# Optimization experiments

Measured on AMD Instinct MI355X. Metric: run time of the kernel, lower is better.

## Reference

```python
import jax, jax.numpy as jnp
import numpy as np

B, S, E, NH = 2, 2048, 1024, 4
HD = E // NH  # 256


def setup_inputs() -> dict:
    key = jax.random.key(0)
    ks = jax.random.split(key, 8)
    return {
        "q": jax.random.normal(ks[0], (B, S, E), jnp.float32),
        "k": jax.random.normal(ks[1], (B, S, E), jnp.float32),
        "v": jax.random.normal(ks[2], (B, S, E), jnp.float32),
        # gate Dense params (kernel zero-init in the module; use small random for a nontrivial baseline)
        "igate_kernel": jax.random.normal(ks[3], (3 * E, NH), jnp.float32) * 0.02,
        "igate_bias": jax.random.normal(ks[4], (NH,), jnp.float32) * 0.1,
        "fgate_kernel": jax.random.normal(ks[5], (3 * E, NH), jnp.float32) * 0.02,
        "fgate_bias": jnp.linspace(3.0, 6.0, NH, dtype=jnp.float32),  # bias_linspace_init
        "rms_scale": jax.random.normal(ks[6], (HD,), jnp.float32) * 0.02,
    }


def _mlstm_head(q, k, v, ig, fg, eps=1e-06):
    # q,k,v: (S, DH); ig, fg: (S, 1)
    s, dh = q.shape
    log_f = jax.nn.log_sigmoid(fg)                       # (S,1)
    cs = jnp.concatenate([jnp.zeros((1, 1), log_f.dtype),
                          jnp.cumsum(log_f, axis=0)], axis=0)  # (S+1,1)
    neg = jnp.asarray(-0.7 * jnp.finfo(cs.dtype).max, cs.dtype)
    log_d = jnp.where(jnp.tri(s, dtype=bool),
                      (cs - cs.T)[1:, 1:] + ig.T, neg)   # (S,S)
    m = jnp.max(log_d, axis=-1, keepdims=True)           # row-wise stabilizer
    d = jnp.exp(log_d - m)
    c = (q @ (k.T / jnp.sqrt(dh))) * d                   # (S,S)
    n = jnp.maximum(jnp.sum(c, axis=-1, keepdims=True), jnp.exp(-m))
    return (c / (n + eps)) @ v                           # (S,DH)


def reference(q, k, v, igate_kernel, igate_bias, fgate_kernel, fgate_bias, rms_scale):
    b, s, e = q.shape
    nh = igate_kernel.shape[1]
    hd = e // nh
    gate_in = jnp.concatenate((q, k, v), axis=-1)                 # (B,S,3E)
    ig = (gate_in @ igate_kernel + igate_bias).swapaxes(-1, -2)[..., None]  # (B,NH,S,1)
    fg = (gate_in @ fgate_kernel + fgate_bias).swapaxes(-1, -2)[..., None]  # (B,NH,S,1)
    qh = q.reshape(b, s, nh, hd).swapaxes(1, 2)                   # (B,NH,S,HD)
    kh = k.reshape(b, s, nh, hd).swapaxes(1, 2)
    vh = v.reshape(b, s, nh, hd).swapaxes(1, 2)
    h = jax.vmap(jax.vmap(_mlstm_head))(qh, kh, vh, ig, fg)      # (B,NH,S,HD)
    # RMSNorm over head_dim with (1+scale)
    var = jnp.mean(jnp.square(h.astype(jnp.float32)), axis=-1, keepdims=True)
    h = (h * jax.lax.rsqrt(var + 1e-06)).astype(h.dtype) * (1.0 + rms_scale)
    return h.swapaxes(1, 2).reshape(b, s, e)
```

## Files before the change

kernel.cpp:

```cpp
#include <hip/hip_runtime.h>
#include <math.h>

static constexpr int B_  = 2;
static constexpr int S_  = 2048;
static constexpr int E_  = 1024;
static constexpr int NH_ = 4;
static constexpr int HD_ = 256;
static constexpr int BH_ = B_ * NH_;

typedef __attribute__((ext_vector_type(8))) _Float16 half8;
typedef __attribute__((ext_vector_type(4))) float    f32x4;
typedef __attribute__((ext_vector_type(4))) _Float16 half4v;

__global__ __launch_bounds__(1024) void prep_kernel(
    const float* __restrict__ q, const float* __restrict__ k, const float* __restrict__ v,
    const float* __restrict__ igk, const float* __restrict__ igb,
    const float* __restrict__ fgk, const float* __restrict__ fgb,
    float* __restrict__ ig_out, float* __restrict__ fg_out,
    _Float16* __restrict__ Qh, _Float16* __restrict__ Kh, _Float16* __restrict__ Vt)
{
    __shared__ __align__(16) char PSM[98304];
    float4* wi = (float4*)PSM;
    float4* wf = wi + 3 * E_;

    const int t = threadIdx.x;
    #pragma unroll
    for (int i = 0; i < 3; ++i) {
        int e = t + 1024 * i;
        wi[e] = ((const float4*)igk)[e];
        wf[e] = ((const float4*)fgk)[e];
    }
    __syncthreads();

    const int wave = t >> 6;
    const int l    = t & 63;
    const int bs   = blockIdx.x * 16 + wave;
    const int b = bs >> 11, s = bs & (S_ - 1);
    const float* qrow = q + (size_t)bs * E_;
    const float* krow = k + (size_t)bs * E_;
    const float* vrow = v + (size_t)bs * E_;

    float accI[4] = {0.f,0.f,0.f,0.f}, accF[4] = {0.f,0.f,0.f,0.f};
    #pragma unroll
    for (int j = 0; j < 48; ++j) {
        const int e = l + 64 * j;
        float g;
        if (j < 16)       g = qrow[e];
        else if (j < 32)  g = krow[e - E_];
        else              g = vrow[e - 2 * E_];
        if (j < 16) {
            int hh = e >> 8, d = e & 255;
            Qh[(((size_t)(b * NH_ + hh)) * S_ + s) * HD_ + d] = (_Float16)(g * 0.0625f);
        } else if (j < 32) {
            int e2 = e - E_; int hh = e2 >> 8, d = e2 & 255;
            Kh[(((size_t)(b * NH_ + hh)) * S_ + s) * HD_ + d] = (_Float16)g;
        }
        float4 wiv = wi[e];
        float4 wfv = wf[e];
        accI[0] = fmaf(g, wiv.x, accI[0]); accI[1] = fmaf(g, wiv.y, accI[1]);
        accI[2] = fmaf(g, wiv.z, accI[2]); accI[3] = fmaf(g, wiv.w, accI[3]);
        accF[0] = fmaf(g, wfv.x, accF[0]); accF[1] = fmaf(g, wfv.y, accF[1]);
        accF[2] = fmaf(g, wfv.z, accF[2]); accF[3] = fmaf(g, wfv.w, accF[3]);
    }
    #pragma unroll
    for (int m = 1; m < 64; m <<= 1) {
        #pragma unroll
        for (int h = 0; h < 4; ++h) {
            accI[h] += __shfl_xor(accI[h], m);
            accF[h] += __shfl_xor(accF[h], m);
        }
    }
    if (l == 0) {
        #pragma unroll
        for (int h = 0; h < 4; ++h) {
            ig_out[((size_t)(b * NH_ + h)) * S_ + s] = accI[h] + igb[h];
            fg_out[((size_t)(b * NH_ + h)) * S_ + s] = accF[h] + fgb[h];
        }
    }

    __syncthreads();
    {
        float (*tile)[65] = (float(*)[65])(PSM + (t >> 8) * 16640);
        const int tid = t & 255;
        const int m  = blockIdx.x * 4 + (t >> 8);
        const int bh = m & 7;
        const int sb = (m >> 3) & 31;
        const int db = m >> 8;
        const int bb = bh >> 2, hh = bh & 3;
        const int j4 = (tid & 15) * 4;
        const int i0 = tid >> 4;
        const float* src = v + ((size_t)(bb * S_ + sb * 64)) * E_ + hh * HD_ + db * 64;
        #pragma unroll
        for (int p = 0; p < 4; ++p) {
            int i = i0 + p * 16;
            float4 val = *(const float4*)(src + (size_t)i * E_ + j4);
            tile[i][j4] = val.x; tile[i][j4+1] = val.y; tile[i][j4+2] = val.z; tile[i][j4+3] = val.w;
        }
        __syncthreads();
        const int s4 = (tid & 15) * 4;
        const int d0 = tid >> 4;
        _Float16* dst = Vt + ((size_t)bh * HD_ + db * 64) * S_ + sb * 64;
        #pragma unroll
        for (int p = 0; p < 4; ++p) {
            int d = d0 + p * 16;
            half4v pk;
            pk.x = (_Float16)tile[s4][d];   pk.y = (_Float16)tile[s4+1][d];
            pk.z = (_Float16)tile[s4+2][d]; pk.w = (_Float16)tile[s4+3][d];
            *(half4v*)(dst + (size_t)d * S_ + s4) = pk;
        }
    }
}

static constexpr int KSS = 264;
static constexpr int VSS = 72;
static constexpr int PBS = 72;
static constexpr int OFF_VS  = 64 * KSS * 2;
static constexpr int OFF_PB  = OFF_VS + 256 * VSS * 2;
static constexpr int OFF_RSE = OFF_PB + 2 * 16 * PBS * 2;
static constexpr int OFF_SSE = OFF_RSE + 512;
static constexpr int OFF_AMM = OFF_SSE + 512;
static constexpr int OFF_G   = OFF_AMM + S_ * 4;
static constexpr int OFF_M   = OFF_G   + S_ * 4;
static constexpr int SMB     = OFF_M   + S_ * 4;

__global__ __launch_bounds__(512, 2) void mlstm_kernel(
    const _Float16* __restrict__ Qh, const _Float16* __restrict__ Kh,
    const _Float16* __restrict__ Vt,
    const float* __restrict__ ig, const float* __restrict__ fg,
    const float* __restrict__ rms_scale, float* __restrict__ out)
{
    __shared__ __align__(16) char SMEM[SMB];
    _Float16* Ks    = (_Float16*)SMEM;
    _Float16* Vs    = (_Float16*)(SMEM + OFF_VS);
    _Float16* Pb    = (_Float16*)(SMEM + OFF_PB);
    float*    rsumE = (float*)(SMEM + OFF_RSE);
    float*    ssE   = (float*)(SMEM + OFF_SSE);
    float*    sAmM  = (float*)(SMEM + OFF_AMM);
    float*    sG    = (float*)(SMEM + OFF_G);
    float*    sM    = (float*)(SMEM + OFF_M);

    const int z  = blockIdx.x;
    const int bh = z & 7;
    const int u  = z >> 3;
    const int b  = bh >> 2, h = bh & 3;
    const int t  = threadIdx.x;
    const int w  = t >> 6;
    const int l  = t & 63;
    const int col  = l & 15;
    const int quad = l >> 4;
    const int qo   = quad * 8;
    const int rw   = w >> 2;
    const int cq   = w & 3;

    {
        float* sc = (float*)SMEM;
        const float* fgp = fg + (size_t)bh * S_;
        const float* igp = ig + (size_t)bh * S_;
        float ls[4];
        float run = 0.f;
        #pragma unroll
        for (int i = 0; i < 4; ++i) {
            float x = fgp[t * 4 + i];
            float lg = (x >= 0.f) ? -log1pf(expf(-x)) : (x - log1pf(expf(x)));
            run += lg;
            ls[i] = run;
        }
        sc[t] = run;
        __syncthreads();
        for (int off = 1; off < 512; off <<= 1) {
            float vv = (t >= off) ? sc[t - off] : 0.f;
            __syncthreads();
            sc[t] += vv;
            __syncthreads();
        }
        float excl = sc[t] - run;
        float A[4], g[4], gm[4];
        #pragma unroll
        for (int i = 0; i < 4; ++i) A[i] = excl + ls[i];
        float rmax = -__builtin_inff();
        #pragma unroll
        for (int i = 0; i < 4; ++i) {
            g[i] = igp[t * 4 + i] - A[i];
            rmax = fmaxf(rmax, g[i]);
            gm[i] = rmax;
        }
        __syncthreads();
        sc[t] = rmax;
        __syncthreads();
        for (int off = 1; off < 512; off <<= 1) {
            float vv = (t >= off) ? sc[t - off] : -__builtin_inff();
            __syncthreads();
            sc[t] = fmaxf(sc[t], vv);
            __syncthreads();
        }
        float exm = (t == 0) ? -__builtin_inff() : sc[t - 1];
        #pragma unroll
        for (int i = 0; i < 4; ++i) {
            float cm = fmaxf(exm, gm[i]);
            float Mi = A[i] + cm;
            sAmM[t * 4 + i] = A[i] - Mi;
            sG[t * 4 + i]   = g[i];
            sM[t * 4 + i]   = Mi;
        }
        __syncthreads();
    }

    const _Float16* Qp  = Qh + (size_t)bh * S_ * HD_;
    const _Float16* Kp  = Kh + (size_t)bh * S_ * HD_;
    const _Float16* Vtp = Vt + (size_t)bh * HD_ * S_;
    _Float16* Pbr = Pb + rw * 16 * PBS;

    half8 kpre[4], vpre[4];
    auto issueK = [&](int c0n) {
        #pragma unroll
        for (int i = 0; i < 4; ++i) {
            int p = t + 512 * i;
            int row = p >> 5, ck = p & 31;
            kpre[i] = *(const half8*)(Kp + (size_t)(c0n + row) * HD_ + ck * 8);
        }
    };
    auto issueV = [&](int c0n) {
        #pragma unroll
        for (int i = 0; i < 4; ++i) {
            int p = t + 512 * i;
            int n = p >> 3, ch = p & 7;
            vpre[i] = *(const half8*)(Vtp + (size_t)n * S_ + c0n + ch * 8);
        }
    };

    issueK(0);
    issueV(0);

    for (int pass = 0; pass < 2; ++pass) {
        const int rb = pass ? (63 - u) : u;
        const int rowbase = rb * 32 + rw * 16;

        half8 qf[8];
        #pragma unroll
        for (int kk = 0; kk < 8; ++kk)
            qf[kk] = *(const half8*)(Qp + (size_t)(rowbase + col) * HD_ + kk * 32 + qo);
        float amM[4];
        #pragma unroll
        for (int rr = 0; rr < 4; ++rr) amM[rr] = sAmM[rowbase + quad * 4 + rr];

        f32x4 acc[4];
        #pragma unroll
        for (int nn = 0; nn < 4; ++nn) acc[nn] = (f32x4){0.f, 0.f, 0.f, 0.f};
        float rs[4] = {0.f, 0.f, 0.f, 0.f};

        const int Tt = (rb >> 1) + 1;
        for (int jt = 0; jt < Tt; ++jt) {
            const int c0 = jt << 6;
            __syncthreads();
            #pragma unroll
            for (int i = 0; i < 4; ++i) {
                int p = t + 512 * i;
                int row = p >> 5, ck = p & 31;
                *(half8*)(Ks + row * KSS + ck * 8) = kpre[i];
            }
            #pragma unroll
            for (int i = 0; i < 4; ++i) {
                int p = t + 512 * i;
                int n = p >> 3, ch = p & 7;
                *(half8*)(Vs + n * VSS + ch * 8) = vpre[i];
            }
            __syncthreads();
            if (!(pass == 1 && jt + 1 == Tt)) {
                const int cn = (jt + 1 < Tt) ? (c0 + 64) : 0;
                issueK(cn);
                issueV(cn);
            }
            const float gv = sG[c0 + cq * 16 + col];
            f32x4 sc0 = (f32x4){0.f,0.f,0.f,0.f};
            #pragma unroll
            for (int kk = 0; kk < 8; ++kk) {
                half8 kf = *(const half8*)(Ks + (cq * 16 + col) * KSS + kk * 32 + qo);
                sc0 = __builtin_amdgcn_mfma_f32_16x16x32_f16(qf[kk], kf, sc0, 0, 0, 0);
            }
            #pragma unroll
            for (int rr = 0; rr < 4; ++rr) {
                const int ig_ = rowbase + quad * 4 + rr;
                float e0 = __expf(amM[rr] + gv);
                float p0 = (c0 + cq * 16 + col <= ig_) ? sc0[rr] * e0 : 0.f;
                rs[rr] += p0;
                Pbr[(quad * 4 + rr) * PBS + cq * 16 + col] = (_Float16)p0;
            }
            __syncthreads();
            half8 af0 = *(const half8*)(Pbr + col * PBS + qo);
            half8 af1 = *(const half8*)(Pbr + col * PBS + 32 + qo);
            #pragma unroll
            for (int nn = 0; nn < 4; ++nn) {
                const int n = cq * 64 + nn * 16 + col;
                half8 vf0 = *(const half8*)(Vs + n * VSS + qo);
                half8 vf1 = *(const half8*)(Vs + n * VSS + 32 + qo);
                acc[nn] = __builtin_amdgcn_mfma_f32_16x16x32_f16(af0, vf0, acc[nn], 0, 0, 0);
                acc[nn] = __builtin_amdgcn_mfma_f32_16x16x32_f16(af1, vf1, acc[nn], 0, 0, 0);
            }
        }

        #pragma unroll
        for (int m = 1; m < 16; m <<= 1) {
            #pragma unroll
            for (int rr = 0; rr < 4; ++rr) rs[rr] += __shfl_xor(rs[rr], m);
        }
        if (col == 0) {
            #pragma unroll
            for (int rr = 0; rr < 4; ++rr)
                rsumE[rw * 64 + cq * 16 + quad * 4 + rr] = rs[rr];
        }
        __syncthreads();
        float inv[4], ss[4];
        #pragma unroll
        for (int rr = 0; rr < 4; ++rr) {
            const int r = quad * 4 + rr;
            float tot = rsumE[rw * 64 + r] + rsumE[rw * 64 + 16 + r]
                      + rsumE[rw * 64 + 32 + r] + rsumE[rw * 64 + 48 + r];
            float Mv = sM[rowbase + r];
            float n = fmaxf(tot, __expf(-Mv)) + 1e-6f;
            inv[rr] = 1.0f / n;
            ss[rr] = 0.f;
        }
        #pragma unroll
        for (int nn = 0; nn < 4; ++nn) {
            #pragma unroll
            for (int rr = 0; rr < 4; ++rr) {
                float hv = acc[nn][rr] * inv[rr];
                acc[nn][rr] = hv;
                ss[rr] = fmaf(hv, hv, ss[rr]);
            }
        }
        #pragma unroll
        for (int m = 1; m < 16; m <<= 1) {
            #pragma unroll
            for (int rr = 0; rr < 4; ++rr) ss[rr] += __shfl_xor(ss[rr], m);
        }
        if (col == 0) {
            #pragma unroll
            for (int rr = 0; rr < 4; ++rr)
                ssE[rw * 64 + cq * 16 + quad * 4 + rr] = ss[rr];
        }
        __syncthreads();
        #pragma unroll
        for (int rr = 0; rr < 4; ++rr) {
            const int r = quad * 4 + rr;
            float sst = ssE[rw * 64 + r] + ssE[rw * 64 + 16 + r]
                      + ssE[rw * 64 + 32 + r] + ssE[rw * 64 + 48 + r];
            float rstd = rsqrtf(sst * (1.0f / HD_) + 1e-6f);
            float* orow = out + ((size_t)(b * S_ + rowbase + r)) * E_ + h * HD_;
            #pragma unroll
            for (int nn = 0; nn < 4; ++nn) {
                const int c = cq * 64 + nn * 16 + col;
                orow[c] = acc[nn][rr] * rstd * (1.0f + rms_scale[c]);
            }
        }
        __syncthreads();
    }
}

extern "C" void kernel_launch(void* const* d_in, const int* in_sizes, int n_in,
                              void* d_out, int out_size, void* d_ws, size_t ws_size,
                              hipStream_t stream) {
    (void)in_sizes; (void)n_in; (void)out_size; (void)ws_size;
    const float* q   = (const float*)d_in[0];
    const float* k   = (const float*)d_in[1];
    const float* v   = (const float*)d_in[2];
    const float* igk = (const float*)d_in[3];
    const float* igb = (const float*)d_in[4];
    const float* fgk = (const float*)d_in[5];
    const float* fgb = (const float*)d_in[6];
    const float* rsc = (const float*)d_in[7];
    float* out = (float*)d_out;

    float* ws  = (float*)d_ws;
    float* ig  = ws;
    float* fg  = ws + (size_t)BH_ * S_;
    _Float16* Qh = (_Float16*)(ws + (size_t)2 * BH_ * S_);
    _Float16* Kh = Qh + (size_t)BH_ * S_ * HD_;
    _Float16* Vt = Kh + (size_t)BH_ * S_ * HD_;

    prep_kernel<<<B_ * S_ / 16, 1024, 0, stream>>>(q, k, v, igk, igb, fgk, fgb,
                                                   ig, fg, Qh, Kh, Vt);
    mlstm_kernel<<<BH_ * 32, 512, 0, stream>>>(Qh, Kh, Vt, ig, fg, rsc, out);
}
```

Measured before the change: 167.9 us.

## Restructure mLSTM tile loop: 128-column tiles, register-direct K/V loads, swizzled P buffer

```diff
diff --git a/kernel.cpp b/kernel.cpp
--- a/kernel.cpp
+++ b/kernel.cpp
@@ -111,17 +111,14 @@
     }
 }
 
-static constexpr int KSS = 264;
-static constexpr int VSS = 72;
-static constexpr int PBS = 72;
-static constexpr int OFF_VS  = 64 * KSS * 2;
-static constexpr int OFF_PB  = OFF_VS + 256 * VSS * 2;
-static constexpr int OFF_RSE = OFF_PB + 2 * 16 * PBS * 2;
-static constexpr int OFF_SSE = OFF_RSE + 512;
-static constexpr int OFF_AMM = OFF_SSE + 512;
+static constexpr int PB_BYTES = 32 * 128 * 2;
+static constexpr int OFF_AMM = 2 * PB_BYTES;
 static constexpr int OFF_G   = OFF_AMM + S_ * 4;
-static constexpr int OFF_M   = OFF_G   + S_ * 4;
-static constexpr int SMB     = OFF_M   + S_ * 4;
+static constexpr int OFF_M   = OFF_G + S_ * 4;
+static constexpr int OFF_RS  = OFF_M + S_ * 4;
+static constexpr int OFF_SS  = OFF_RS + 8 * 32 * 4;
+static constexpr int OFF_WR  = OFF_SS + 8 * 32 * 4;
+static constexpr int SMB     = OFF_WR + 64;
 
 __global__ __launch_bounds__(512, 2) void mlstm_kernel(
     const _Float16* __restrict__ Qh, const _Float16* __restrict__ Kh,
@@ -130,14 +127,14 @@
     const float* __restrict__ rms_scale, float* __restrict__ out)
 {
     __shared__ __align__(16) char SMEM[SMB];
-    _Float16* Ks    = (_Float16*)SMEM;
-    _Float16* Vs    = (_Float16*)(SMEM + OFF_VS);
-    _Float16* Pb    = (_Float16*)(SMEM + OFF_PB);
-    float*    rsumE = (float*)(SMEM + OFF_RSE);
-    float*    ssE   = (float*)(SMEM + OFF_SSE);
-    float*    sAmM  = (float*)(SMEM + OFF_AMM);
-    float*    sG    = (float*)(SMEM + OFF_G);
-    float*    sM    = (float*)(SMEM + OFF_M);
+    char*  Pb    = SMEM;
+    float* sAmM  = (float*)(SMEM + OFF_AMM);
+    float* sG    = (float*)(SMEM + OFF_G);
+    float* sM    = (float*)(SMEM + OFF_M);
+    float* rsumP = (float*)(SMEM + OFF_RS);
+    float* ssP   = (float*)(SMEM + OFF_SS);
+    float* wred  = (float*)(SMEM + OFF_WR);
+    float* wred2 = wred + 8;
 
     const int z  = blockIdx.x;
     const int bh = z & 7;
@@ -149,51 +146,55 @@
     const int col  = l & 15;
     const int quad = l >> 4;
     const int qo   = quad * 8;
-    const int rw   = w >> 2;
-    const int cq   = w & 3;
 
     {
-        float* sc = (float*)SMEM;
         const float* fgp = fg + (size_t)bh * S_;
         const float* igp = ig + (size_t)bh * S_;
+        float4 fx = *(const float4*)(fgp + t * 4);
+        float4 ix = *(const float4*)(igp + t * 4);
+        float xi[4] = {fx.x, fx.y, fx.z, fx.w};
+        float gi[4] = {ix.x, ix.y, ix.z, ix.w};
         float ls[4];
         float run = 0.f;
         #pragma unroll
         for (int i = 0; i < 4; ++i) {
-            float x = fgp[t * 4 + i];
+            float x = xi[i];
             float lg = (x >= 0.f) ? -log1pf(expf(-x)) : (x - log1pf(expf(x)));
             run += lg;
             ls[i] = run;
         }
-        sc[t] = run;
-        __syncthreads();
-        for (int off = 1; off < 512; off <<= 1) {
-            float vv = (t >= off) ? sc[t - off] : 0.f;
-            __syncthreads();
-            sc[t] += vv;
-            __syncthreads();
-        }
-        float excl = sc[t] - run;
+        const float own = run;
+        #pragma unroll
+        for (int m = 1; m < 64; m <<= 1) {
+            float o = __shfl_up(run, m);
+            if (l >= m) run += o;
+        }
+        if (l == 63) wred[w] = run;
+        __syncthreads();
+        float wpre = 0.f;
+        for (int ww = 0; ww < w; ++ww) wpre += wred[ww];
+        const float exclT = wpre + run - own;
         float A[4], g[4], gm[4];
-        #pragma unroll
-        for (int i = 0; i < 4; ++i) A[i] = excl + ls[i];
         float rmax = -__builtin_inff();
         #pragma unroll
         for (int i = 0; i < 4; ++i) {
-            g[i] = igp[t * 4 + i] - A[i];
+            A[i] = exclT + ls[i];
+            g[i] = gi[i] - A[i];
             rmax = fmaxf(rmax, g[i]);
             gm[i] = rmax;
         }
-        __syncthreads();
-        sc[t] = rmax;
-        __syncthreads();
-        for (int off = 1; off < 512; off <<= 1) {
-            float vv = (t >= off) ? sc[t - off] : -__builtin_inff();
-            __syncthreads();
-            sc[t] = fmaxf(sc[t], vv);
-            __syncthreads();
-        }
-        float exm = (t == 0) ? -__builtin_inff() : sc[t - 1];
+        float sm = rmax;
+        #pragma unroll
+        for (int m = 1; m < 64; m <<= 1) {
+            float o = __shfl_up(sm, m);
+            if (l >= m) sm = fmaxf(sm, o);
+        }
+        if (l == 63) wred2[w] = sm;
+        __syncthreads();
+        float exm = -__builtin_inff();
+        for (int ww = 0; ww < w; ++ww) exm = fmaxf(exm, wred2[ww]);
+        float up = __shfl_up(sm, 1);
+        if (l > 0) exm = fmaxf(exm, up);
         #pragma unroll
         for (int i = 0; i < 4; ++i) {
             float cm = fmaxf(exm, gm[i]);
@@ -208,150 +209,176 @@
     const _Float16* Qp  = Qh + (size_t)bh * S_ * HD_;
     const _Float16* Kp  = Kh + (size_t)bh * S_ * HD_;
     const _Float16* Vtp = Vt + (size_t)bh * HD_ * S_;
-    _Float16* Pbr = Pb + rw * 16 * PBS;
-
-    half8 kpre[4], vpre[4];
-    auto issueK = [&](int c0n) {
-        #pragma unroll
-        for (int i = 0; i < 4; ++i) {
-            int p = t + 512 * i;
-            int row = p >> 5, ck = p & 31;
-            kpre[i] = *(const half8*)(Kp + (size_t)(c0n + row) * HD_ + ck * 8);
-        }
-    };
-    auto issueV = [&](int c0n) {
-        #pragma unroll
-        for (int i = 0; i < 4; ++i) {
-            int p = t + 512 * i;
-            int n = p >> 3, ch = p & 7;
-            vpre[i] = *(const half8*)(Vtp + (size_t)n * S_ + c0n + ch * 8);
-        }
-    };
-
-    issueK(0);
-    issueV(0);
+
+    const float rsc0 = 1.f + rms_scale[w * 32 + col];
+    const float rsc1 = 1.f + rms_scale[w * 32 + 16 + col];
+
+    int buf = 0;
 
     for (int pass = 0; pass < 2; ++pass) {
         const int rb = pass ? (63 - u) : u;
-        const int rowbase = rb * 32 + rw * 16;
-
-        half8 qf[8];
+        const int rowbase = rb * 32;
+        const int Tt = (rb >> 2) + 1;
+
+        half8 qf0[8], qf1[8];
+        #pragma unroll
+        for (int kk = 0; kk < 8; ++kk) {
+            qf0[kk] = *(const half8*)(Qp + (size_t)(rowbase + col) * HD_ + kk * 32 + qo);
+            qf1[kk] = *(const half8*)(Qp + (size_t)(rowbase + 16 + col) * HD_ + kk * 32 + qo);
+        }
+        float amM0[4], amM1[4];
+        #pragma unroll
+        for (int rr = 0; rr < 4; ++rr) {
+            amM0[rr] = sAmM[rowbase + quad * 4 + rr];
+            amM1[rr] = sAmM[rowbase + 16 + quad * 4 + rr];
+        }
+
+        f32x4 acc[4];
+        #pragma unroll
+        for (int i = 0; i < 4; ++i) acc[i] = (f32x4){0.f, 0.f, 0.f, 0.f};
+        float rs0[4] = {0.f,0.f,0.f,0.f}, rs1[4] = {0.f,0.f,0.f,0.f};
+
+        const _Float16* kcol_base = Kp + (size_t)(w * 16 + col) * HD_ + qo;
+        half8 kf[8];
         #pragma unroll
         for (int kk = 0; kk < 8; ++kk)
-            qf[kk] = *(const half8*)(Qp + (size_t)(rowbase + col) * HD_ + kk * 32 + qo);
-        float amM[4];
-        #pragma unroll
-        for (int rr = 0; rr < 4; ++rr) amM[rr] = sAmM[rowbase + quad * 4 + rr];
-
-        f32x4 acc[4];
-        #pragma unroll
-        for (int nn = 0; nn < 4; ++nn) acc[nn] = (f32x4){0.f, 0.f, 0.f, 0.f};
-        float rs[4] = {0.f, 0.f, 0.f, 0.f};
-
-        const int Tt = (rb >> 1) + 1;
+            kf[kk] = *(const half8*)(kcol_base + kk * 32);
+
+        half8 vf[8];
         for (int jt = 0; jt < Tt; ++jt) {
-            const int c0 = jt << 6;
+            const int c0 = jt << 7;
+            #pragma unroll
+            for (int nsub = 0; nsub < 2; ++nsub) {
+                #pragma unroll
+                for (int kh = 0; kh < 4; ++kh)
+                    vf[nsub * 4 + kh] = *(const half8*)(Vtp
+                        + (size_t)(w * 32 + nsub * 16 + col) * S_ + c0 + kh * 32 + qo);
+            }
+            f32x4 sc0 = (f32x4){0.f,0.f,0.f,0.f}, sc1 = (f32x4){0.f,0.f,0.f,0.f};
+            #pragma unroll
+            for (int kk = 0; kk < 8; ++kk) {
+                sc0 = __builtin_amdgcn_mfma_f32_16x16x32_f16(qf0[kk], kf[kk], sc0, 0, 0, 0);
+                sc1 = __builtin_amdgcn_mfma_f32_16x16x32_f16(qf1[kk], kf[kk], sc1, 0, 0, 0);
+            }
+            if (jt + 1 < Tt) {
+                const _Float16* kb = kcol_base + (size_t)(c0 + 128) * HD_;
+                #pragma unroll
+                for (int kk = 0; kk < 8; ++kk)
+                    kf[kk] = *(const half8*)(kb + kk * 32);
+            }
+            const int gcol = c0 + w * 16 + col;
+            const float gv = sG[gcol];
+            char* pbC = Pb + buf * PB_BYTES;
+            const int hcb = (w * 16 + col) << 1;
+            #pragma unroll
+            for (int rr = 0; rr < 4; ++rr) {
+                const int r0 = quad * 4 + rr;
+                const int sw = (r0 & 7) << 4;
+                float e0 = __expf(amM0[rr] + gv);
+                float p0 = (gcol <= rowbase + r0) ? sc0[rr] * e0 : 0.f;
+                rs0[rr] += p0;
+                *(_Float16*)(pbC + (((r0 << 8) + hcb) ^ sw)) = (_Float16)p0;
+                float e1 = __expf(amM1[rr] + gv);
+                float p1 = (gcol <= rowbase + 16 + r0) ? sc1[rr] * e1 : 0.f;
+                rs1[rr] += p1;
+                const int r1 = r0 + 16;
+                *(_Float16*)(pbC + (((r1 << 8) + hcb) ^ sw)) = (_Float16)p1;
+            }
             __syncthreads();
             #pragma unroll
-            for (int i = 0; i < 4; ++i) {
-                int p = t + 512 * i;
-                int row = p >> 5, ck = p & 31;
-                *(half8*)(Ks + row * KSS + ck * 8) = kpre[i];
-            }
-            #pragma unroll
-            for (int i = 0; i < 4; ++i) {
-                int p = t + 512 * i;
-                int n = p >> 3, ch = p & 7;
-                *(half8*)(Vs + n * VSS + ch * 8) = vpre[i];
-            }
-            __syncthreads();
-            if (!(pass == 1 && jt + 1 == Tt)) {
-                const int cn = (jt + 1 < Tt) ? (c0 + 64) : 0;
-                issueK(cn);
-                issueV(cn);
-            }
-            const float gv = sG[c0 + cq * 16 + col];
-            f32x4 sc0 = (f32x4){0.f,0.f,0.f,0.f};
-            #pragma unroll
-            for (int kk = 0; kk < 8; ++kk) {
-                half8 kf = *(const half8*)(Ks + (cq * 16 + col) * KSS + kk * 32 + qo);
-                sc0 = __builtin_amdgcn_mfma_f32_16x16x32_f16(qf[kk], kf, sc0, 0, 0, 0);
-            }
-            #pragma unroll
-            for (int rr = 0; rr < 4; ++rr) {
-                const int ig_ = rowbase + quad * 4 + rr;
-                float e0 = __expf(amM[rr] + gv);
-                float p0 = (c0 + cq * 16 + col <= ig_) ? sc0[rr] * e0 : 0.f;
-                rs[rr] += p0;
-                Pbr[(quad * 4 + rr) * PBS + cq * 16 + col] = (_Float16)p0;
-            }
-            __syncthreads();
-            half8 af0 = *(const half8*)(Pbr + col * PBS + qo);
-            half8 af1 = *(const half8*)(Pbr + col * PBS + 32 + qo);
-            #pragma unroll
-            for (int nn = 0; nn < 4; ++nn) {
-                const int n = cq * 64 + nn * 16 + col;
-                half8 vf0 = *(const half8*)(Vs + n * VSS + qo);
-                half8 vf1 = *(const half8*)(Vs + n * VSS + 32 + qo);
-                acc[nn] = __builtin_amdgcn_mfma_f32_16x16x32_f16(af0, vf0, acc[nn], 0, 0, 0);
-                acc[nn] = __builtin_amdgcn_mfma_f32_16x16x32_f16(af1, vf1, acc[nn], 0, 0, 0);
-            }
+            for (int rsub = 0; rsub < 2; ++rsub) {
+                const int prow = rsub * 16 + col;
+                half8 af[4];
+                #pragma unroll
+                for (int kh = 0; kh < 4; ++kh)
+                    af[kh] = *(const half8*)(pbC
+                        + ((prow << 8) + ((kh * 64 + qo * 2) ^ ((col & 7) << 4))));
+                #pragma unroll
+                for (int kh = 0; kh < 4; ++kh) {
+                    acc[rsub * 2 + 0] = __builtin_amdgcn_mfma_f32_16x16x32_f16(af[kh], vf[kh],     acc[rsub * 2 + 0], 0, 0, 0);
+                    acc[rsub * 2 + 1] = __builtin_amdgcn_mfma_f32_16x16x32_f16(af[kh], vf[4 + kh], acc[rsub * 2 + 1], 0, 0, 0);
+                }
+            }
+            buf ^= 1;
         }
 
         #pragma unroll
         for (int m = 1; m < 16; m <<= 1) {
             #pragma unroll
-            for (int rr = 0; rr < 4; ++rr) rs[rr] += __shfl_xor(rs[rr], m);
+            for (int rr = 0; rr < 4; ++rr) {
+                rs0[rr] += __shfl_xor(rs0[rr], m);
+                rs1[rr] += __shfl_xor(rs1[rr], m);
+            }
         }
         if (col == 0) {
             #pragma unroll
-            for (int rr = 0; rr < 4; ++rr)
-                rsumE[rw * 64 + cq * 16 + quad * 4 + rr] = rs[rr];
-        }
-        __syncthreads();
-        float inv[4], ss[4];
+            for (int rr = 0; rr < 4; ++rr) {
+                rsumP[w * 32 + quad * 4 + rr]      = rs0[rr];
+                rsumP[w * 32 + 16 + quad * 4 + rr] = rs1[rr];
+            }
+        }
+        __syncthreads();
+        float inv0[4], inv1[4];
         #pragma unroll
         for (int rr = 0; rr < 4; ++rr) {
-            const int r = quad * 4 + rr;
-            float tot = rsumE[rw * 64 + r] + rsumE[rw * 64 + 16 + r]
-                      + rsumE[rw * 64 + 32 + r] + rsumE[rw * 64 + 48 + r];
-            float Mv = sM[rowbase + r];
-            float n = fmaxf(tot, __expf(-Mv)) + 1e-6f;
-            inv[rr] = 1.0f / n;
-            ss[rr] = 0.f;
-        }
-        #pragma unroll
-        for (int nn = 0; nn < 4; ++nn) {
-            #pragma unroll
-            for (int rr = 0; rr < 4; ++rr) {
-                float hv = acc[nn][rr] * inv[rr];
-                acc[nn][rr] = hv;
-                ss[rr] = fmaf(hv, hv, ss[rr]);
+            const int r0 = quad * 4 + rr;
+            float tot0 = 0.f, tot1 = 0.f;
+            #pragma unroll
+            for (int ww = 0; ww < 8; ++ww) {
+                tot0 += rsumP[ww * 32 + r0];
+                tot1 += rsumP[ww * 32 + 16 + r0];
+            }
+            float M0 = sM[rowbase + r0];
+            float M1 = sM[rowbase + 16 + r0];
+            inv0[rr] = 1.0f / (fmaxf(tot0, __expf(-M0)) + 1e-6f);
+            inv1[rr] = 1.0f / (fmaxf(tot1, __expf(-M1)) + 1e-6f);
+        }
+        float ss0[4] = {0.f,0.f,0.f,0.f}, ss1[4] = {0.f,0.f,0.f,0.f};
+        #pragma unroll
+        for (int nsub = 0; nsub < 2; ++nsub) {
+            #pragma unroll
+            for (int rr = 0; rr < 4; ++rr) {
+                float h0 = acc[nsub][rr] * inv0[rr];
+                acc[nsub][rr] = h0;
+                ss0[rr] = fmaf(h0, h0, ss0[rr]);
+                float h1 = acc[2 + nsub][rr] * inv1[rr];
+                acc[2 + nsub][rr] = h1;
+                ss1[rr] = fmaf(h1, h1, ss1[rr]);
             }
         }
         #pragma unroll
         for (int m = 1; m < 16; m <<= 1) {
             #pragma unroll
-            for (int rr = 0; rr < 4; ++rr) ss[rr] += __shfl_xor(ss[rr], m);
+            for (int rr = 0; rr < 4; ++rr) {
+                ss0[rr] += __shfl_xor(ss0[rr], m);
+                ss1[rr] += __shfl_xor(ss1[rr], m);
+            }
         }
         if (col == 0) {
             #pragma unroll
-            for (int rr = 0; rr < 4; ++rr)
-                ssE[rw * 64 + cq * 16 + quad * 4 + rr] = ss[rr];
+            for (int rr = 0; rr < 4; ++rr) {
+                ssP[w * 32 + quad * 4 + rr]      = ss0[rr];
+                ssP[w * 32 + 16 + quad * 4 + rr] = ss1[rr];
+            }
         }
         __syncthreads();
         #pragma unroll
         for (int rr = 0; rr < 4; ++rr) {
-            const int r = quad * 4 + rr;
-            float sst = ssE[rw * 64 + r] + ssE[rw * 64 + 16 + r]
-                      + ssE[rw * 64 + 32 + r] + ssE[rw * 64 + 48 + r];
-            float rstd = rsqrtf(sst * (1.0f / HD_) + 1e-6f);
-            float* orow = out + ((size_t)(b * S_ + rowbase + r)) * E_ + h * HD_;
-            #pragma unroll
-            for (int nn = 0; nn < 4; ++nn) {
-                const int c = cq * 64 + nn * 16 + col;
-                orow[c] = acc[nn][rr] * rstd * (1.0f + rms_scale[c]);
-            }
+            const int r0 = quad * 4 + rr;
+            float sst0 = 0.f, sst1 = 0.f;
+            #pragma unroll
+            for (int ww = 0; ww < 8; ++ww) {
+                sst0 += ssP[ww * 32 + r0];
+                sst1 += ssP[ww * 32 + 16 + r0];
+            }
+            float rstd0 = rsqrtf(sst0 * (1.0f / HD_) + 1e-6f);
+            float rstd1 = rsqrtf(sst1 * (1.0f / HD_) + 1e-6f);
+            float* o0 = out + ((size_t)(b * S_ + rowbase + r0)) * E_ + h * HD_ + w * 32;
+            float* o1 = out + ((size_t)(b * S_ + rowbase + 16 + r0)) * E_ + h * HD_ + w * 32;
+            o0[col]      = acc[0][rr] * rstd0 * rsc0;
+            o0[16 + col] = acc[1][rr] * rstd0 * rsc1;
+            o1[col]      = acc[2][rr] * rstd1 * rsc0;
+            o1[16 + col] = acc[3][rr] * rstd1 * rsc1;
         }
         __syncthreads();
     }
```

Result: slower. 184.6 us (+9.9%).
